# Kernel tuning notes

Measured on AMD Instinct MI355X. Metric: run time of the kernel, lower is better.

The kernel has to match this reference:

```python
import jax, jax.numpy as jnp
import numpy as np

IN_F = 2048
OUT_F = 2048
BS = 64  # block_size
NIB = IN_F // BS   # 32 in-blocks
NOB = OUT_F // BS  # 32 out-blocks


def setup_inputs() -> dict:
    key = jax.random.key(0)
    k_x, k_s1, k_s2, k_m = jax.random.split(key, 4)
    bound = 1.0 / np.sqrt(BS)
    x = jax.random.normal(k_x, (4, 4096, IN_F), dtype=jnp.float32)
    stage1 = jax.random.uniform(k_s1, (NIB * BS, BS), minval=-bound, maxval=bound, dtype=jnp.float32)
    stage2 = jax.random.uniform(k_s2, (NOB * BS, BS), minval=-bound, maxval=bound, dtype=jnp.float32)
    mix_w = jax.random.normal(k_m, (NOB * BS, NIB * BS), dtype=jnp.float32) / np.sqrt(IN_F)
    return {"x": x, "stage1": stage1, "stage2": stage2, "mix_w": mix_w}


def _blockdiag(x, weight, num_blocks):
    # x: [..., num_blocks*BS]; weight: [num_blocks*BS, BS] viewed as [g, c, d]
    shape = x.shape[:-1]
    xg = x.reshape(-1, num_blocks, BS)
    w = weight.reshape(num_blocks, BS, BS)
    y = jnp.einsum('ngc,gcd->ngd', xg, w)
    return y.reshape(*shape, num_blocks * BS)


def _shuffle(x):
    # interpret last dim as [BS, NIB], transpose to [NIB, BS]
    shape = x.shape[:-1]
    return x.reshape(-1, BS, NIB).transpose(0, 2, 1).reshape(*shape, NIB * BS)


def reference(x, stage1, stage2, mix_w):
    h = _blockdiag(x, stage1, NIB)          # [B,S,IN_F]
    h = _shuffle(h)                          # [B,S,IN_F]
    h = jnp.einsum('bsi,oi->bso', h, mix_w)  # dense mix, no bias
    return _blockdiag(h, stage2, NOB)        # [B,S,OUT_F]
```

## Files before the change

kernel.cpp:

```cpp
#include <hip/hip_runtime.h>
#include <stdint.h>

#define IN_F 2048
#define OUT_F 2048
#define MTOK 16384

typedef __attribute__((ext_vector_type(8))) __bf16 bf16x8;
typedef __attribute__((ext_vector_type(4))) float f32x4;
typedef __attribute__((ext_vector_type(4))) unsigned short us4;

typedef const __attribute__((address_space(1))) void g_void;
typedef __attribute__((address_space(3))) void l_void;

__device__ __forceinline__ void async16(void* lds, const void* g) {
    __builtin_amdgcn_global_load_lds((g_void*)(uintptr_t)g, (l_void*)(uintptr_t)lds, 16, 0, 0);
}

__device__ __forceinline__ unsigned short f2bf(float x) {
    union { float f; uint32_t u; } v; v.f = x;
    uint32_t r = v.u + 0x7fffu + ((v.u >> 16) & 1u);
    return (unsigned short)(r >> 16);
}

__global__ void k_permute_mixw(const float* __restrict__ W, unsigned short* __restrict__ Bp) {
    __shared__ float row[2112];
    const int t = threadIdx.x;
    const float* src = W + (size_t)blockIdx.x * IN_F;
#pragma unroll
    for (int q = 0; q < 2; ++q) {
        int id4 = q * 256 + t;
        float4 v = *(const float4*)(src + id4 * 4);
        int i = id4 * 4;
        int b = i + (i >> 5);
        row[b] = v.x; row[b + 1] = v.y; row[b + 2] = v.z; row[b + 3] = v.w;
    }
    __syncthreads();
    unsigned short* dst = Bp + (size_t)blockIdx.x * IN_F;
#pragma unroll
    for (int q = 0; q < 8; ++q) {
        int j = q * 256 + t;
        int i = ((j & 31) << 6) | (j >> 5);
        dst[j] = f2bf(row[i + (i >> 5)]);
    }
}

__global__ void k_transpose_stages(const float* __restrict__ s1, const float* __restrict__ s2,
                                   unsigned short* __restrict__ W1T, unsigned short* __restrict__ W2T) {
    __shared__ float tile[64 * 65];
    const int b = blockIdx.x;
    const float* src = (b < 32 ? s1 : s2) + (size_t)(b & 31) * 4096;
    unsigned short* dst = (b < 32 ? W1T : W2T) + (size_t)(b & 31) * 4096;
    const int t = threadIdx.x;
#pragma unroll
    for (int q = 0; q < 16; ++q) {
        int id = q * 256 + t;
        tile[(id >> 6) * 65 + (id & 63)] = src[id];
    }
    __syncthreads();
#pragma unroll
    for (int q = 0; q < 16; ++q) {
        int id = q * 256 + t;
        int d = id >> 6, c = id & 63;
        dst[id] = f2bf(tile[c * 65 + d]);
    }
}

__global__ __launch_bounds__(256, 2) void k_stage1(
    const float* __restrict__ X, const unsigned short* __restrict__ W1T,
    unsigned short* __restrict__ H) {
    __shared__ unsigned short smem[128 * 64 + 64 * 64];
    unsigned short* Xs = smem;
    unsigned short* Ws = smem + 128 * 64;
    const int t = threadIdx.x;
    const int lane = t & 63, wave = t >> 6;
    const int quad = lane >> 4, l16 = lane & 15;
    const int m0 = blockIdx.x * 128;
    const int g = blockIdx.y;

    const unsigned short* Wg = W1T + g * 4096;
    async16((char*)Ws + t * 16, Wg + t * 8);
    async16((char*)Ws + 4096 + t * 16, Wg + 2048 + t * 8);

    const float* Xg = X + (size_t)m0 * IN_F + g * 64;
#pragma unroll
    for (int q = 0; q < 8; ++q) {
        int id = q * 256 + t;
        int r = id >> 4, c4 = id & 15;
        float4 v = *(const float4*)(Xg + (size_t)r * IN_F + c4 * 4);
        us4 b; b.x = f2bf(v.x); b.y = f2bf(v.y); b.z = f2bf(v.z); b.w = f2bf(v.w);
        *(us4*)(Xs + r * 64 + c4 * 4) = b;
    }
    __syncthreads();

    f32x4 acc[2][4];
#pragma unroll
    for (int i = 0; i < 2; ++i)
#pragma unroll
        for (int j = 0; j < 4; ++j) acc[i][j] = (f32x4)0.f;

#pragma unroll
    for (int ks = 0; ks < 2; ++ks) {
        bf16x8 af[2], bfr[4];
#pragma unroll
        for (int i = 0; i < 2; ++i)
            af[i] = *(const bf16x8*)(Xs + (wave * 32 + i * 16 + l16) * 64 + ks * 32 + quad * 8);
#pragma unroll
        for (int j = 0; j < 4; ++j)
            bfr[j] = *(const bf16x8*)(Ws + (j * 16 + l16) * 64 + ks * 32 + quad * 8);
#pragma unroll
        for (int i = 0; i < 2; ++i)
#pragma unroll
            for (int j = 0; j < 4; ++j)
                acc[i][j] = __builtin_amdgcn_mfma_f32_16x16x32_bf16(af[i], bfr[j], acc[i][j], 0, 0, 0);
    }

#pragma unroll
    for (int i = 0; i < 2; ++i)
#pragma unroll
        for (int j = 0; j < 4; ++j)
#pragma unroll
            for (int r = 0; r < 4; ++r) {
                int m = m0 + wave * 32 + i * 16 + quad * 4 + r;
                int col = g * 64 + j * 16 + l16;
                H[(size_t)m * IN_F + col] = f2bf(acc[i][j][r]);
            }
}

__global__ __launch_bounds__(256, 2) void k_mix_gemm(
    const unsigned short* __restrict__ A, const unsigned short* __restrict__ B,
    const unsigned short* __restrict__ W2T, float* __restrict__ C) {
    __shared__ unsigned short smem[16384];
    unsigned short* As = smem;
    unsigned short* Bs = smem + 8192;
    const int t = threadIdx.x;
    const int lane = t & 63, wave = t >> 6;
    const int quad = lane >> 4, l16 = lane & 15;
    const int mw = wave & 1, nw = wave >> 1;
    const int m0 = blockIdx.x * 128;
    const int n0 = blockIdx.y * 128;
    const int rr = t >> 3, chunk = t & 7;

    f32x4 acc[4][4];
#pragma unroll
    for (int i = 0; i < 4; ++i)
#pragma unroll
        for (int j = 0; j < 4; ++j) acc[i][j] = (f32x4)0.f;

    for (int kb = 0; kb < IN_F; kb += 64) {
#pragma unroll
        for (int q = 0; q < 4; ++q) {
            int r = q * 32 + rr;
            async16((char*)As + (size_t)(q * 4096 + t * 16),
                    A + (size_t)(m0 + r) * IN_F + kb + chunk * 8);
            async16((char*)Bs + (size_t)(q * 4096 + t * 16),
                    B + (size_t)(n0 + r) * IN_F + kb + chunk * 8);
        }
        __syncthreads();
#pragma unroll
        for (int ks = 0; ks < 2; ++ks) {
            bf16x8 af[4], bfr[4];
#pragma unroll
            for (int i = 0; i < 4; ++i)
                af[i] = *(const bf16x8*)(As + (mw * 64 + i * 16 + l16) * 64 + ks * 32 + quad * 8);
#pragma unroll
            for (int j = 0; j < 4; ++j)
                bfr[j] = *(const bf16x8*)(Bs + (nw * 64 + j * 16 + l16) * 64 + ks * 32 + quad * 8);
#pragma unroll
            for (int i = 0; i < 4; ++i)
#pragma unroll
                for (int j = 0; j < 4; ++j)
                    acc[i][j] = __builtin_amdgcn_mfma_f32_16x16x32_bf16(af[i], bfr[j], acc[i][j], 0, 0, 0);
        }
        __syncthreads();
    }

    unsigned short* P = smem + wave * 4096;
#pragma unroll
    for (int i = 0; i < 4; ++i)
#pragma unroll
        for (int j = 0; j < 4; ++j)
#pragma unroll
            for (int r = 0; r < 4; ++r)
                P[(i * 16 + quad * 4 + r) * 64 + j * 16 + l16] = f2bf(acc[i][j][r]);

    const int g = (n0 >> 6) + nw;
    const unsigned short* W2g = W2T + g * 4096;
    bf16x8 wb[4][2];
#pragma unroll
    for (int j = 0; j < 4; ++j)
#pragma unroll
        for (int ks = 0; ks < 2; ++ks)
            wb[j][ks] = *(const bf16x8*)(W2g + (j * 16 + l16) * 64 + ks * 32 + quad * 8);

#pragma unroll
    for (int i = 0; i < 4; ++i) {
        bf16x8 pa0 = *(const bf16x8*)(P + (i * 16 + l16) * 64 + quad * 8);
        bf16x8 pa1 = *(const bf16x8*)(P + (i * 16 + l16) * 64 + 32 + quad * 8);
#pragma unroll
        for (int j = 0; j < 4; ++j) {
            f32x4 o = (f32x4)0.f;
            o = __builtin_amdgcn_mfma_f32_16x16x32_bf16(pa0, wb[j][0], o, 0, 0, 0);
            o = __builtin_amdgcn_mfma_f32_16x16x32_bf16(pa1, wb[j][1], o, 0, 0, 0);
            float* Cp = C + (size_t)(m0 + mw * 64 + i * 16 + quad * 4) * OUT_F
                          + (n0 + nw * 64 + j * 16 + l16);
#pragma unroll
            for (int r = 0; r < 4; ++r) Cp[(size_t)r * OUT_F] = o[r];
        }
    }
}

extern "C" void kernel_launch(void* const* d_in, const int* in_sizes, int n_in,
                              void* d_out, int out_size, void* d_ws, size_t ws_size,
                              hipStream_t stream) {
    const float* x  = (const float*)d_in[0];
    const float* s1 = (const float*)d_in[1];
    const float* s2 = (const float*)d_in[2];
    const float* mw = (const float*)d_in[3];
    float* out = (float*)d_out;

    char* ws = (char*)d_ws;
    unsigned short* hA  = (unsigned short*)ws;
    unsigned short* Bp  = (unsigned short*)(ws + (size_t)MTOK * IN_F * 2);
    unsigned short* W1T = (unsigned short*)(ws + (size_t)MTOK * IN_F * 2
                                               + (size_t)OUT_F * IN_F * 2);
    unsigned short* W2T = W1T + 32 * 4096;

    k_permute_mixw<<<2048, 256, 0, stream>>>(mw, Bp);
    k_transpose_stages<<<64, 256, 0, stream>>>(s1, s2, W1T, W2T);
    k_stage1<<<dim3(128, 32), 256, 0, stream>>>(x, W1T, hA);
    k_mix_gemm<<<dim3(128, 16), 256, 0, stream>>>(hA, Bp, W2T, out);
}
```

Before: 434.4 us.

## Swizzle LDS tiles to avoid bank conflicts and coalesce stage1 output stores

In the mix GEMM, the async global-to-LDS loads now fetch XOR-swizzled 16-byte chunks, and the fragment reads use the matching swizzle. The epilogue staging buffer P is swizzled the same way. Both are meant to remove LDS bank conflicts on the row-major 64-wide tiles. In stage1, the tiles are padded to a stride of 72 to avoid conflicts, and results are staged through LDS so H is written with 16-byte coalesced row stores instead of scattered 2-byte stores. The cost is an extra barrier and an LDS round trip in stage1, and the weight load there becomes a synchronous copy.

```diff
diff --git a/kernel.cpp b/kernel.cpp
--- a/kernel.cpp
+++ b/kernel.cpp
@@ -8,6 +8,7 @@
 typedef __attribute__((ext_vector_type(8))) __bf16 bf16x8;
 typedef __attribute__((ext_vector_type(4))) float f32x4;
 typedef __attribute__((ext_vector_type(4))) unsigned short us4;
+typedef __attribute__((ext_vector_type(8))) unsigned short us8;
 
 typedef const __attribute__((address_space(1))) void g_void;
 typedef __attribute__((address_space(3))) void l_void;
@@ -65,12 +66,12 @@
     }
 }
 
+#define XS_LD 72
 __global__ __launch_bounds__(256, 2) void k_stage1(
     const float* __restrict__ X, const unsigned short* __restrict__ W1T,
     unsigned short* __restrict__ H) {
-    __shared__ unsigned short smem[128 * 64 + 64 * 64];
-    unsigned short* Xs = smem;
-    unsigned short* Ws = smem + 128 * 64;
+    __shared__ unsigned short Xs[128 * XS_LD];
+    __shared__ unsigned short Ws[64 * XS_LD];
     const int t = threadIdx.x;
     const int lane = t & 63, wave = t >> 6;
     const int quad = lane >> 4, l16 = lane & 15;
@@ -78,8 +79,13 @@
     const int g = blockIdx.y;
 
     const unsigned short* Wg = W1T + g * 4096;
-    async16((char*)Ws + t * 16, Wg + t * 8);
-    async16((char*)Ws + 4096 + t * 16, Wg + 2048 + t * 8);
+#pragma unroll
+    for (int p = 0; p < 2; ++p) {
+        int id = p * 256 + t;
+        int r = id >> 3, c = id & 7;
+        us8 v = *(const us8*)(Wg + r * 64 + c * 8);
+        *(us8*)(Ws + r * XS_LD + c * 8) = v;
+    }
 
     const float* Xg = X + (size_t)m0 * IN_F + g * 64;
 #pragma unroll
@@ -88,7 +94,7 @@
         int r = id >> 4, c4 = id & 15;
         float4 v = *(const float4*)(Xg + (size_t)r * IN_F + c4 * 4);
         us4 b; b.x = f2bf(v.x); b.y = f2bf(v.y); b.z = f2bf(v.z); b.w = f2bf(v.w);
-        *(us4*)(Xs + r * 64 + c4 * 4) = b;
+        *(us4*)(Xs + r * XS_LD + c4 * 4) = b;
     }
     __syncthreads();
 
@@ -103,10 +109,10 @@
         bf16x8 af[2], bfr[4];
 #pragma unroll
         for (int i = 0; i < 2; ++i)
-            af[i] = *(const bf16x8*)(Xs + (wave * 32 + i * 16 + l16) * 64 + ks * 32 + quad * 8);
+            af[i] = *(const bf16x8*)(Xs + (wave * 32 + i * 16 + l16) * XS_LD + ks * 32 + quad * 8);
 #pragma unroll
         for (int j = 0; j < 4; ++j)
-            bfr[j] = *(const bf16x8*)(Ws + (j * 16 + l16) * 64 + ks * 32 + quad * 8);
+            bfr[j] = *(const bf16x8*)(Ws + (j * 16 + l16) * XS_LD + ks * 32 + quad * 8);
 #pragma unroll
         for (int i = 0; i < 2; ++i)
 #pragma unroll
@@ -114,16 +120,23 @@
                 acc[i][j] = __builtin_amdgcn_mfma_f32_16x16x32_bf16(af[i], bfr[j], acc[i][j], 0, 0, 0);
     }
 
+    __syncthreads();
+    unsigned short* Hs = Xs;
 #pragma unroll
     for (int i = 0; i < 2; ++i)
 #pragma unroll
         for (int j = 0; j < 4; ++j)
 #pragma unroll
-            for (int r = 0; r < 4; ++r) {
-                int m = m0 + wave * 32 + i * 16 + quad * 4 + r;
-                int col = g * 64 + j * 16 + l16;
-                H[(size_t)m * IN_F + col] = f2bf(acc[i][j][r]);
-            }
+            for (int r = 0; r < 4; ++r)
+                Hs[(wave * 32 + i * 16 + quad * 4 + r) * 64 + j * 16 + l16] = f2bf(acc[i][j][r]);
+    __syncthreads();
+#pragma unroll
+    for (int p = 0; p < 4; ++p) {
+        int id = p * 256 + t;
+        int r = id >> 3, c = id & 7;
+        us8 v = *(const us8*)(Hs + r * 64 + c * 8);
+        *(us8*)(H + (size_t)(m0 + r) * IN_F + g * 64 + c * 8) = v;
+    }
 }
 
 __global__ __launch_bounds__(256, 2) void k_mix_gemm(
@@ -139,6 +152,8 @@
     const int m0 = blockIdx.x * 128;
     const int n0 = blockIdx.y * 128;
     const int rr = t >> 3, chunk = t & 7;
+    const int gsw = (chunk ^ (rr & 7)) * 8;
+    const int lsw = l16 & 7;
 
     f32x4 acc[4][4];
 #pragma unroll
@@ -151,9 +166,9 @@
         for (int q = 0; q < 4; ++q) {
             int r = q * 32 + rr;
             async16((char*)As + (size_t)(q * 4096 + t * 16),
-                    A + (size_t)(m0 + r) * IN_F + kb + chunk * 8);
+                    A + (size_t)(m0 + r) * IN_F + kb + gsw);
             async16((char*)Bs + (size_t)(q * 4096 + t * 16),
-                    B + (size_t)(n0 + r) * IN_F + kb + chunk * 8);
+                    B + (size_t)(n0 + r) * IN_F + kb + gsw);
         }
         __syncthreads();
 #pragma unroll
@@ -161,10 +176,12 @@
             bf16x8 af[4], bfr[4];
 #pragma unroll
             for (int i = 0; i < 4; ++i)
-                af[i] = *(const bf16x8*)(As + (mw * 64 + i * 16 + l16) * 64 + ks * 32 + quad * 8);
+                af[i] = *(const bf16x8*)(As + (mw * 64 + i * 16 + l16) * 64
+                                            + (((ks * 4 + quad) ^ lsw) * 8));
 #pragma unroll
             for (int j = 0; j < 4; ++j)
-                bfr[j] = *(const bf16x8*)(Bs + (nw * 64 + j * 16 + l16) * 64 + ks * 32 + quad * 8);
+                bfr[j] = *(const bf16x8*)(Bs + (nw * 64 + j * 16 + l16) * 64
+                                             + (((ks * 4 + quad) ^ lsw) * 8));
 #pragma unroll
             for (int i = 0; i < 4; ++i)
 #pragma unroll
@@ -178,10 +195,15 @@
 #pragma unroll
     for (int i = 0; i < 4; ++i)
 #pragma unroll
-        for (int j = 0; j < 4; ++j)
-#pragma unroll
-            for (int r = 0; r < 4; ++r)
-                P[(i * 16 + quad * 4 + r) * 64 + j * 16 + l16] = f2bf(acc[i][j][r]);
+        for (int j = 0; j < 4; ++j) {
+            int cc = j * 2 + (l16 >> 3);
+            int ci = l16 & 7;
+#pragma unroll
+            for (int r = 0; r < 4; ++r) {
+                int pr = i * 16 + quad * 4 + r;
+                P[pr * 64 + ((cc ^ (pr & 7)) * 8) + ci] = f2bf(acc[i][j][r]);
+            }
+        }
 
     const int g = (n0 >> 6) + nw;
     const unsigned short* W2g = W2T + g * 4096;
@@ -194,8 +216,8 @@
 
 #pragma unroll
     for (int i = 0; i < 4; ++i) {
-        bf16x8 pa0 = *(const bf16x8*)(P + (i * 16 + l16) * 64 + quad * 8);
-        bf16x8 pa1 = *(const bf16x8*)(P + (i * 16 + l16) * 64 + 32 + quad * 8);
+        bf16x8 pa0 = *(const bf16x8*)(P + (i * 16 + l16) * 64 + ((quad ^ lsw) * 8));
+        bf16x8 pa1 = *(const bf16x8*)(P + (i * 16 + l16) * 64 + (((4 + quad) ^ lsw) * 8));
 #pragma unroll
         for (int j = 0; j < 4; ++j) {
             f32x4 o = (f32x4)0.f;
```

Measured after the change: 399.9 us. 1.09x faster.
